# Kernel tuning notes

Measured on AMD Instinct MI355X. Metric: run time of the kernel, lower is better.

## Reference

```python
import jax, jax.numpy as jnp
import numpy as np

# 8 directional difference stencils (N, S, E, W, NE, SE, SW, NW), OIHW [8,1,3,3]
_WINDOWS = np.array([
    [[0, 1, 0], [0, -1, 0], [0, 0, 0]],
    [[0, 0, 0], [0, -1, 0], [0, 1, 0]],
    [[0, 0, 0], [0, -1, 1], [0, 0, 0]],
    [[0, 0, 0], [1, -1, 0], [0, 0, 0]],
    [[0, 0, 1], [0, -1, 0], [0, 0, 0]],
    [[0, 0, 0], [0, -1, 0], [0, 0, 1]],
    [[0, 0, 0], [0, -1, 0], [1, 0, 0]],
    [[1, 0, 0], [0, -1, 0], [0, 0, 0]],
], dtype=np.float32).reshape(8, 1, 3, 3)

ITERATIONS = 30  # int(self.iterations.item()) with init value 30.0


def setup_inputs() -> dict:
    key = jax.random.key(0)
    k1, k2, k3 = jax.random.split(key, 3)
    x = jax.random.normal(k1, (32, 3, 512, 512), dtype=jnp.float32)
    W_expand = jax.random.normal(k2, (3, 3, 1, 1), dtype=jnp.float32) * 0.3
    b_expand = jax.random.normal(k3, (3,), dtype=jnp.float32) * 0.1
    return {
        "x": x,
        "delta": jnp.float32(0.1),
        "kappa": jnp.float32(15.0),
        "W_expand": W_expand,
        "b_expand": b_expand,
    }


def reference(x, delta, kappa, W_expand, b_expand):
    K = jnp.asarray(_WINDOWS)  # [8,1,3,3]
    # axial directions weight 1, diagonal directions weight 1/(sqrt(2))^2 = 0.5
    dir_w = jnp.array([1.0, 1.0, 1.0, 1.0, 0.5, 0.5, 0.5, 0.5],
                      dtype=x.dtype).reshape(1, 8, 1, 1)

    # RGB -> luminance, [B,1,H,W]
    u = (0.299 * x[:, 0] + 0.587 * x[:, 1] + 0.114 * x[:, 2])[:, None]

    def step(u, _):
        # all 8 directional gradients in one grouped conv: [B,8,H,W]
        nabla = jax.lax.conv_general_dilated(
            u, K, window_strides=(1, 1), padding='SAME',
            dimension_numbers=('NCHW', 'OIHW', 'NCHW'))
        diff = 1.0 / (1.0 + (nabla / kappa) ** 2)  # Perona-Malik diffusivity
        upd = jnp.sum(dir_w * diff * nabla, axis=1, keepdims=True)
        return u + delta * upd, None

    u, _ = jax.lax.scan(step, u, None, length=ITERATIONS)

    # repeat to 3 channels then 1x1 conv (expand_channels)
    u_rgb = jnp.repeat(u, 3, axis=1)  # [B,3,H,W]
    out = jnp.einsum('oi,bihw->bohw', W_expand[:, :, 0, 0], u_rgb)
    out = out + b_expand[None, :, None, None]
    return out
```

## Files before the change

kernel.cpp:

```cpp
#include <hip/hip_runtime.h>

#define BATCH 32
#define HGT 512
#define WID 512
#define PLANE (HGT * WID)
#define NPIX (BATCH * PLANE)
#define BSTRIDE (3 * PLANE)
#define NQUAD (NPIX / 4)

#define RSLAB 32
#define SLABS (HGT / RSLAB)
#define FBLOCKS (BATCH * SLABS)
#define FT 512
#define NW 8

__device__ __forceinline__ float4 ld4(const float* p) {
    return *reinterpret_cast<const float4*>(p);
}
__device__ __forceinline__ void st4(float* p, float4 v) {
    *reinterpret_cast<float4*>(p) = v;
}

__device__ __forceinline__ float pm_flux(float d, float ik2) {
    return d * __builtin_amdgcn_rcpf(fmaf(d * d, ik2, 1.f));
}

__device__ __forceinline__ void level_flux(const float a[6], const float b[6],
                                           float vF[4], float seF[5], float swF[5],
                                           float ik2) {
#pragma unroll
    for (int j = 0; j < 4; ++j) vF[j] = pm_flux(b[j + 1] - a[j + 1], ik2);
#pragma unroll
    for (int i = 0; i < 5; ++i) seF[i] = pm_flux(b[i + 1] - a[i], ik2);
#pragma unroll
    for (int i = 0; i < 5; ++i) swF[i] = pm_flux(b[i] - a[i + 1], ik2);
}

__device__ __forceinline__ void load_row2(const float* __restrict__ buf, int row, int o,
                                          float rA[6], float rB[6]) {
    const float* p = buf + row * WID + (o << 2);
    float4 a = ld4(p);
    float4 b = ld4(p + 256);
    float aW63 = __shfl(a.w, 63);
    float bX0  = __shfl(b.x, 0);
    float lA   = __shfl_up(a.w, 1);
    float rAr  = __shfl_down(a.x, 1);
    float lB   = __shfl_up(b.w, 1);
    float rBr  = __shfl_down(b.x, 1);
    rA[0] = (o == 0) ? 0.f : lA;
    rA[1] = a.x; rA[2] = a.y; rA[3] = a.z; rA[4] = a.w;
    rA[5] = (o == 63) ? bX0 : rAr;
    rB[0] = (o == 0) ? aW63 : lB;
    rB[1] = b.x; rB[2] = b.y; rB[3] = b.z; rB[4] = b.w;
    rB[5] = (o == 63) ? 0.f : rBr;
}

struct SegState {
    float m[6];
    float pV[4], pSE[5], pSW[5];
};

__device__ __forceinline__ void seg_init(SegState& S_, const float a6[6],
                                         const float m6[6], float ik2) {
#pragma unroll
    for (int t = 0; t < 6; ++t) S_.m[t] = m6[t];
    level_flux(a6, m6, S_.pV, S_.pSE, S_.pSW, ik2);
}

__device__ __forceinline__ float4 seg_step(SegState& S_, const float d6[6],
                                           float delta, float ik2) {
    float hF[5];
#pragma unroll
    for (int t = 0; t < 5; ++t) hF[t] = pm_flux(S_.m[t + 1] - S_.m[t], ik2);
    float cV[4], cSE[5], cSW[5];
    level_flux(S_.m, d6, cV, cSE, cSW, ik2);
    float o[4];
#pragma unroll
    for (int j = 0; j < 4; ++j) {
        float axial = cV[j] - S_.pV[j] + hF[j + 1] - hF[j];
        float diag  = cSE[j + 1] + cSW[j] - S_.pSE[j] - S_.pSW[j + 1];
        o[j] = fmaf(delta, fmaf(0.5f, diag, axial), S_.m[j + 1]);
    }
#pragma unroll
    for (int t = 0; t < 6; ++t) S_.m[t] = d6[t];
#pragma unroll
    for (int j = 0; j < 4; ++j) S_.pV[j] = cV[j];
#pragma unroll
    for (int t = 0; t < 5; ++t) { S_.pSE[t] = cSE[t]; S_.pSW[t] = cSW[t]; }
    return make_float4(o[0], o[1], o[2], o[3]);
}

template <int MODE, int S>
__global__ __launch_bounds__(FT, 4)
void pm_fusedk(const float* __restrict__ src, int sstr,
               float* __restrict__ dst, int dstr,
               const float* __restrict__ pdelta, const float* __restrict__ pkappa,
               const float* __restrict__ Wexp, const float* __restrict__ bexp) {
    constexpr int LR = RSLAB + 2 * S;
    __shared__ float buf[LR * WID];

    const int img   = blockIdx.x >> 4;
    const int slab  = blockIdx.x & (SLABS - 1);
    const int H0    = slab * RSLAB;
    const int tid   = threadIdx.x;
    const int strip = tid >> 6;
    const int o     = tid & 63;

    const float delta = *pdelta;
    const float kappa = *pkappa;
    const float ik2 = __builtin_amdgcn_rcpf(kappa * kappa);

    const float* sb = src + (size_t)img * sstr;
    for (int i = tid; i < LR * (WID / 4); i += FT) {
        int row = i >> 7;
        int q   = i & 127;
        int g = H0 - S + row;
        float4 v = make_float4(0.f, 0.f, 0.f, 0.f);
        if ((unsigned)g < (unsigned)HGT) {
            const float* p = sb + g * WID + (q << 2);
            if (MODE == 0) {
                float4 r = ld4(p), gg = ld4(p + PLANE), bb = ld4(p + 2 * PLANE);
                v.x = fmaf(0.299f, r.x, fmaf(0.587f, gg.x, 0.114f * bb.x));
                v.y = fmaf(0.299f, r.y, fmaf(0.587f, gg.y, 0.114f * bb.y));
                v.z = fmaf(0.299f, r.z, fmaf(0.587f, gg.z, 0.114f * bb.z));
                v.w = fmaf(0.299f, r.w, fmaf(0.587f, gg.w, 0.114f * bb.w));
            } else {
                v = ld4(p);
            }
        }
        st4(buf + row * WID + (q << 2), v);
    }
    __syncthreads();

    float s0c = 0.f, s1c = 0.f, s2c = 0.f, b0c = 0.f, b1c = 0.f, b2c = 0.f;
    if (MODE == 2) {
        s0c = Wexp[0] + Wexp[1] + Wexp[2];
        s1c = Wexp[3] + Wexp[4] + Wexp[5];
        s2c = Wexp[6] + Wexp[7] + Wexp[8];
        b0c = bexp[0]; b1c = bexp[1]; b2c = bexp[2];
    }

    float* db = dst + (size_t)img * dstr;

    for (int s = 0; s < S; ++s) {
        const int tot = LR - 2 - 2 * s;
        const int bse = tot >> 3, rem = tot & 7;
        const int n   = bse + (strip < rem ? 1 : 0);
        const int st0 = s + 1 + strip * bse + (strip < rem ? strip : rem);
        const bool fin = (s == S - 1);

        SegState SA, SB;
        {
            float a6[6], b6[6], mA[6], mB[6];
            load_row2(buf, st0 - 1, o, a6, b6);
            load_row2(buf, st0, o, mA, mB);
            seg_init(SA, a6, mA, ik2);
            seg_init(SB, b6, mB, ik2);
        }
        float4 fA = make_float4(0, 0, 0, 0), fB = fA, lA4 = fA, lB4 = fA;

        for (int i = 0; i < n; ++i) {
            float dA[6], dB[6];
            load_row2(buf, st0 + i + 1, o, dA, dB);
            float4 rA = seg_step(SA, dA, delta, ik2);
            float4 rB = seg_step(SB, dB, delta, ik2);
            const int g = H0 - S + st0 + i;
            if ((unsigned)g >= (unsigned)HGT) {
                rA = make_float4(0, 0, 0, 0);
                rB = make_float4(0, 0, 0, 0);
            }
            if (fin) {
                float* p = db + (size_t)g * WID + (o << 2);
                if (MODE == 2) {
                    st4(p, make_float4(fmaf(s0c, rA.x, b0c), fmaf(s0c, rA.y, b0c),
                                       fmaf(s0c, rA.z, b0c), fmaf(s0c, rA.w, b0c)));
                    st4(p + 256, make_float4(fmaf(s0c, rB.x, b0c), fmaf(s0c, rB.y, b0c),
                                             fmaf(s0c, rB.z, b0c), fmaf(s0c, rB.w, b0c)));
                    st4(p + PLANE,
                        make_float4(fmaf(s1c, rA.x, b1c), fmaf(s1c, rA.y, b1c),
                                    fmaf(s1c, rA.z, b1c), fmaf(s1c, rA.w, b1c)));
                    st4(p + PLANE + 256,
                        make_float4(fmaf(s1c, rB.x, b1c), fmaf(s1c, rB.y, b1c),
                                    fmaf(s1c, rB.z, b1c), fmaf(s1c, rB.w, b1c)));
                    st4(p + 2 * PLANE,
                        make_float4(fmaf(s2c, rA.x, b2c), fmaf(s2c, rA.y, b2c),
                                    fmaf(s2c, rA.z, b2c), fmaf(s2c, rA.w, b2c)));
                    st4(p + 2 * PLANE + 256,
                        make_float4(fmaf(s2c, rB.x, b2c), fmaf(s2c, rB.y, b2c),
                                    fmaf(s2c, rB.z, b2c), fmaf(s2c, rB.w, b2c)));
                } else {
                    st4(p, rA);
                    st4(p + 256, rB);
                }
            } else if (i == 0) {
                fA = rA; fB = rB;
            } else if (i == n - 1) {
                lA4 = rA; lB4 = rB;
            } else {
                float* p = buf + (st0 + i) * WID + (o << 2);
                st4(p, rA);
                st4(p + 256, rB);
            }
        }
        if (!fin) {
            __syncthreads();
            {
                float* p = buf + st0 * WID + (o << 2);
                st4(p, fA);
                st4(p + 256, fB);
            }
            {
                float* p = buf + (st0 + n - 1) * WID + (o << 2);
                st4(p, lA4);
                st4(p + 256, lB4);
            }
            __syncthreads();
        }
    }
}

__global__ void expand_from(const float* __restrict__ usrc, int ustr,
                            float* __restrict__ out,
                            const float* __restrict__ Wexp,
                            const float* __restrict__ bexp) {
    int idx = blockIdx.x * blockDim.x + threadIdx.x;
    if (idx >= NQUAD) return;
    int b = idx / (PLANE / 4);
    int off = (idx - b * (PLANE / 4)) * 4;

    float4 u = ld4(usrc + (size_t)b * ustr + off);
    float s0 = Wexp[0] + Wexp[1] + Wexp[2];
    float s1 = Wexp[3] + Wexp[4] + Wexp[5];
    float s2 = Wexp[6] + Wexp[7] + Wexp[8];
    float b0 = bexp[0], b1 = bexp[1], b2 = bexp[2];

    size_t base = (size_t)b * BSTRIDE + off;
    st4(out + base, make_float4(fmaf(s0, u.x, b0), fmaf(s0, u.y, b0),
                                fmaf(s0, u.z, b0), fmaf(s0, u.w, b0)));
    st4(out + base + PLANE, make_float4(fmaf(s1, u.x, b1), fmaf(s1, u.y, b1),
                                        fmaf(s1, u.z, b1), fmaf(s1, u.w, b1)));
    st4(out + base + 2 * PLANE, make_float4(fmaf(s2, u.x, b2), fmaf(s2, u.y, b2),
                                            fmaf(s2, u.z, b2), fmaf(s2, u.w, b2)));
}

extern "C" void kernel_launch(void* const* d_in, const int* in_sizes, int n_in,
                              void* d_out, int out_size, void* d_ws, size_t ws_size,
                              hipStream_t stream) {
    const float* x      = (const float*)d_in[0];
    const float* pdelta = (const float*)d_in[1];
    const float* pkappa = (const float*)d_in[2];
    const float* Wexp   = (const float*)d_in[3];
    const float* bexp   = (const float*)d_in[4];
    float* out = (float*)d_out;

    const size_t need = (size_t)2 * NPIX * sizeof(float);
    if (ws_size >= need) {
        float* uA = (float*)d_ws;
        float* uB = uA + NPIX;
        pm_fusedk<0, 4><<<FBLOCKS, FT, 0, stream>>>(
            x, BSTRIDE, uA, PLANE, pdelta, pkappa, Wexp, bexp);
        float* s = uA;
        float* d = uB;
        for (int k = 0; k < 6; ++k) {
            pm_fusedk<1, 4><<<FBLOCKS, FT, 0, stream>>>(
                s, PLANE, d, PLANE, pdelta, pkappa, Wexp, bexp);
            float* t = s; s = d; d = t;
        }
        pm_fusedk<2, 2><<<FBLOCKS, FT, 0, stream>>>(
            s, PLANE, out, BSTRIDE, pdelta, pkappa, Wexp, bexp);
    } else {
        float* uA = out;
        float* uB = out + PLANE;
        pm_fusedk<0, 4><<<FBLOCKS, FT, 0, stream>>>(
            x, BSTRIDE, uA, BSTRIDE, pdelta, pkappa, Wexp, bexp);
        float* s = uA;
        float* d = uB;
        for (int k = 0; k < 6; ++k) {
            pm_fusedk<1, 4><<<FBLOCKS, FT, 0, stream>>>(
                s, BSTRIDE, d, BSTRIDE, pdelta, pkappa, Wexp, bexp);
            float* t = s; s = d; d = t;
        }
        pm_fusedk<1, 2><<<FBLOCKS, FT, 0, stream>>>(
            s, BSTRIDE, d, BSTRIDE, pdelta, pkappa, Wexp, bexp);
        const int block = 256;
        const int grid_q = (NQUAD + block - 1) / block;
        expand_from<<<grid_q, block, 0, stream>>>(d, BSTRIDE, out, Wexp, bexp);
    }
}
```

Measured before the change: 395.9 us.

## Give each lane 8 contiguous columns and ping-pong row state buffers

Each lane now handles 8 contiguous pixels per row instead of two 4-pixel segments 256 columns apart. This cuts the per-row shuffles to two and shares horizontal flux work across a wider run of pixels. The row loop is unrolled by two, alternating two state structs so no register copies are needed. Launch bounds become an explicit waves-per-EU attribute. The stride-8 LDS float4 accesses may cause bank conflicts, and the wider per-thread state raises register pressure.

```diff
diff --git a/kernel.cpp b/kernel.cpp
--- a/kernel.cpp
+++ b/kernel.cpp
@@ -25,73 +25,37 @@
     return d * __builtin_amdgcn_rcpf(fmaf(d * d, ik2, 1.f));
 }
 
-__device__ __forceinline__ void level_flux(const float a[6], const float b[6],
-                                           float vF[4], float seF[5], float swF[5],
-                                           float ik2) {
-#pragma unroll
-    for (int j = 0; j < 4; ++j) vF[j] = pm_flux(b[j + 1] - a[j + 1], ik2);
-#pragma unroll
-    for (int i = 0; i < 5; ++i) seF[i] = pm_flux(b[i + 1] - a[i], ik2);
-#pragma unroll
-    for (int i = 0; i < 5; ++i) swF[i] = pm_flux(b[i] - a[i + 1], ik2);
-}
-
-__device__ __forceinline__ void load_row2(const float* __restrict__ buf, int row, int o,
-                                          float rA[6], float rB[6]) {
-    const float* p = buf + row * WID + (o << 2);
-    float4 a = ld4(p);
-    float4 b = ld4(p + 256);
-    float aW63 = __shfl(a.w, 63);
-    float bX0  = __shfl(b.x, 0);
-    float lA   = __shfl_up(a.w, 1);
-    float rAr  = __shfl_down(a.x, 1);
-    float lB   = __shfl_up(b.w, 1);
-    float rBr  = __shfl_down(b.x, 1);
-    rA[0] = (o == 0) ? 0.f : lA;
-    rA[1] = a.x; rA[2] = a.y; rA[3] = a.z; rA[4] = a.w;
-    rA[5] = (o == 63) ? bX0 : rAr;
-    rB[0] = (o == 0) ? aW63 : lB;
-    rB[1] = b.x; rB[2] = b.y; rB[3] = b.z; rB[4] = b.w;
-    rB[5] = (o == 63) ? 0.f : rBr;
-}
-
-struct SegState {
-    float m[6];
-    float pV[4], pSE[5], pSW[5];
+struct RowState {
+    float m[10];
+    float pV[8], pSE[9], pSW[9];
 };
 
-__device__ __forceinline__ void seg_init(SegState& S_, const float a6[6],
-                                         const float m6[6], float ik2) {
-#pragma unroll
-    for (int t = 0; t < 6; ++t) S_.m[t] = m6[t];
-    level_flux(a6, m6, S_.pV, S_.pSE, S_.pSW, ik2);
-}
-
-__device__ __forceinline__ float4 seg_step(SegState& S_, const float d6[6],
-                                           float delta, float ik2) {
-    float hF[5];
-#pragma unroll
-    for (int t = 0; t < 5; ++t) hF[t] = pm_flux(S_.m[t + 1] - S_.m[t], ik2);
-    float cV[4], cSE[5], cSW[5];
-    level_flux(S_.m, d6, cV, cSE, cSW, ik2);
-    float o[4];
-#pragma unroll
-    for (int j = 0; j < 4; ++j) {
-        float axial = cV[j] - S_.pV[j] + hF[j + 1] - hF[j];
-        float diag  = cSE[j + 1] + cSW[j] - S_.pSE[j] - S_.pSW[j + 1];
-        o[j] = fmaf(delta, fmaf(0.5f, diag, axial), S_.m[j + 1]);
-    }
-#pragma unroll
-    for (int t = 0; t < 6; ++t) S_.m[t] = d6[t];
-#pragma unroll
-    for (int j = 0; j < 4; ++j) S_.pV[j] = cV[j];
-#pragma unroll
-    for (int t = 0; t < 5; ++t) { S_.pSE[t] = cSE[t]; S_.pSW[t] = cSW[t]; }
-    return make_float4(o[0], o[1], o[2], o[3]);
+__device__ __forceinline__ void load_row10(const float* __restrict__ buf, int row, int o,
+                                           float m[10]) {
+    const float* p = buf + row * WID + (o << 3);
+    float4 lo = ld4(p);
+    float4 hi = ld4(p + 4);
+    float le = __shfl_up(hi.w, 1);
+    float re = __shfl_down(lo.x, 1);
+    m[0] = (o == 0) ? 0.f : le;
+    m[1] = lo.x; m[2] = lo.y; m[3] = lo.z; m[4] = lo.w;
+    m[5] = hi.x; m[6] = hi.y; m[7] = hi.z; m[8] = hi.w;
+    m[9] = (o == 63) ? 0.f : re;
+}
+
+__device__ __forceinline__ void level10(const float a[10], const float b[10],
+                                        float vF[8], float seF[9], float swF[9],
+                                        float ik2) {
+#pragma unroll
+    for (int j = 0; j < 8; ++j) vF[j] = pm_flux(b[j + 1] - a[j + 1], ik2);
+#pragma unroll
+    for (int i = 0; i < 9; ++i) seF[i] = pm_flux(b[i + 1] - a[i], ik2);
+#pragma unroll
+    for (int i = 0; i < 9; ++i) swF[i] = pm_flux(b[i] - a[i + 1], ik2);
 }
 
 template <int MODE, int S>
-__global__ __launch_bounds__(FT, 4)
+__global__ __launch_bounds__(FT) __attribute__((amdgpu_waves_per_eu(4, 4)))
 void pm_fusedk(const float* __restrict__ src, int sstr,
                float* __restrict__ dst, int dstr,
                const float* __restrict__ pdelta, const float* __restrict__ pkappa,
@@ -99,12 +63,12 @@
     constexpr int LR = RSLAB + 2 * S;
     __shared__ float buf[LR * WID];
 
-    const int img   = blockIdx.x >> 4;
-    const int slab  = blockIdx.x & (SLABS - 1);
-    const int H0    = slab * RSLAB;
-    const int tid   = threadIdx.x;
-    const int strip = tid >> 6;
-    const int o     = tid & 63;
+    const int img  = blockIdx.x >> 4;
+    const int slab = blockIdx.x & (SLABS - 1);
+    const int H0   = slab * RSLAB;
+    const int tid  = threadIdx.x;
+    const int wave = tid >> 6;
+    const int o    = tid & 63;
 
     const float delta = *pdelta;
     const float kappa = *pkappa;
@@ -145,75 +109,87 @@
     for (int s = 0; s < S; ++s) {
         const int tot = LR - 2 - 2 * s;
         const int bse = tot >> 3, rem = tot & 7;
-        const int n   = bse + (strip < rem ? 1 : 0);
-        const int st0 = s + 1 + strip * bse + (strip < rem ? strip : rem);
+        const int n   = bse + (wave < rem ? 1 : 0);
+        const int st0 = s + 1 + wave * bse + (wave < rem ? wave : rem);
         const bool fin = (s == S - 1);
 
-        SegState SA, SB;
+        RowState A, B;
         {
-            float a6[6], b6[6], mA[6], mB[6];
-            load_row2(buf, st0 - 1, o, a6, b6);
-            load_row2(buf, st0, o, mA, mB);
-            seg_init(SA, a6, mA, ik2);
-            seg_init(SB, b6, mB, ik2);
-        }
-        float4 fA = make_float4(0, 0, 0, 0), fB = fA, lA4 = fA, lB4 = fA;
-
-        for (int i = 0; i < n; ++i) {
-            float dA[6], dB[6];
-            load_row2(buf, st0 + i + 1, o, dA, dB);
-            float4 rA = seg_step(SA, dA, delta, ik2);
-            float4 rB = seg_step(SB, dB, delta, ik2);
+            float a10[10];
+            load_row10(buf, st0 - 1, o, a10);
+            load_row10(buf, st0, o, A.m);
+            level10(a10, A.m, A.pV, A.pSE, A.pSW, ik2);
+        }
+        float4 f0 = make_float4(0, 0, 0, 0), f1 = f0, l0 = f0, l1 = f0;
+
+        auto do_row = [&](RowState& CUR, RowState& NEXT, int i) {
+            load_row10(buf, st0 + i + 1, o, NEXT.m);
+            float hF[9];
+#pragma unroll
+            for (int t = 0; t < 9; ++t) hF[t] = pm_flux(CUR.m[t + 1] - CUR.m[t], ik2);
+            level10(CUR.m, NEXT.m, NEXT.pV, NEXT.pSE, NEXT.pSW, ik2);
+            float o8[8];
+#pragma unroll
+            for (int j = 0; j < 8; ++j) {
+                float axial = NEXT.pV[j] - CUR.pV[j] + hF[j + 1] - hF[j];
+                float diag  = NEXT.pSE[j + 1] + NEXT.pSW[j]
+                            - CUR.pSE[j] - CUR.pSW[j + 1];
+                o8[j] = fmaf(delta, fmaf(0.5f, diag, axial), CUR.m[j + 1]);
+            }
             const int g = H0 - S + st0 + i;
             if ((unsigned)g >= (unsigned)HGT) {
-                rA = make_float4(0, 0, 0, 0);
-                rB = make_float4(0, 0, 0, 0);
-            }
+#pragma unroll
+                for (int j = 0; j < 8; ++j) o8[j] = 0.f;
+            }
+            float4 r0 = make_float4(o8[0], o8[1], o8[2], o8[3]);
+            float4 r1 = make_float4(o8[4], o8[5], o8[6], o8[7]);
             if (fin) {
-                float* p = db + (size_t)g * WID + (o << 2);
+                float* p = db + (size_t)g * WID + (o << 3);
                 if (MODE == 2) {
-                    st4(p, make_float4(fmaf(s0c, rA.x, b0c), fmaf(s0c, rA.y, b0c),
-                                       fmaf(s0c, rA.z, b0c), fmaf(s0c, rA.w, b0c)));
-                    st4(p + 256, make_float4(fmaf(s0c, rB.x, b0c), fmaf(s0c, rB.y, b0c),
-                                             fmaf(s0c, rB.z, b0c), fmaf(s0c, rB.w, b0c)));
+                    st4(p, make_float4(fmaf(s0c, r0.x, b0c), fmaf(s0c, r0.y, b0c),
+                                       fmaf(s0c, r0.z, b0c), fmaf(s0c, r0.w, b0c)));
+                    st4(p + 4, make_float4(fmaf(s0c, r1.x, b0c), fmaf(s0c, r1.y, b0c),
+                                           fmaf(s0c, r1.z, b0c), fmaf(s0c, r1.w, b0c)));
                     st4(p + PLANE,
-                        make_float4(fmaf(s1c, rA.x, b1c), fmaf(s1c, rA.y, b1c),
-                                    fmaf(s1c, rA.z, b1c), fmaf(s1c, rA.w, b1c)));
-                    st4(p + PLANE + 256,
-                        make_float4(fmaf(s1c, rB.x, b1c), fmaf(s1c, rB.y, b1c),
-                                    fmaf(s1c, rB.z, b1c), fmaf(s1c, rB.w, b1c)));
+                        make_float4(fmaf(s1c, r0.x, b1c), fmaf(s1c, r0.y, b1c),
+                                    fmaf(s1c, r0.z, b1c), fmaf(s1c, r0.w, b1c)));
+                    st4(p + PLANE + 4,
+                        make_float4(fmaf(s1c, r1.x, b1c), fmaf(s1c, r1.y, b1c),
+                                    fmaf(s1c, r1.z, b1c), fmaf(s1c, r1.w, b1c)));
                     st4(p + 2 * PLANE,
-                        make_float4(fmaf(s2c, rA.x, b2c), fmaf(s2c, rA.y, b2c),
-                                    fmaf(s2c, rA.z, b2c), fmaf(s2c, rA.w, b2c)));
-                    st4(p + 2 * PLANE + 256,
-                        make_float4(fmaf(s2c, rB.x, b2c), fmaf(s2c, rB.y, b2c),
-                                    fmaf(s2c, rB.z, b2c), fmaf(s2c, rB.w, b2c)));
+                        make_float4(fmaf(s2c, r0.x, b2c), fmaf(s2c, r0.y, b2c),
+                                    fmaf(s2c, r0.z, b2c), fmaf(s2c, r0.w, b2c)));
+                    st4(p + 2 * PLANE + 4,
+                        make_float4(fmaf(s2c, r1.x, b2c), fmaf(s2c, r1.y, b2c),
+                                    fmaf(s2c, r1.z, b2c), fmaf(s2c, r1.w, b2c)));
                 } else {
-                    st4(p, rA);
-                    st4(p + 256, rB);
+                    st4(p, r0);
+                    st4(p + 4, r1);
                 }
             } else if (i == 0) {
-                fA = rA; fB = rB;
+                f0 = r0; f1 = r1;
             } else if (i == n - 1) {
-                lA4 = rA; lB4 = rB;
+                l0 = r0; l1 = r1;
             } else {
-                float* p = buf + (st0 + i) * WID + (o << 2);
-                st4(p, rA);
-                st4(p + 256, rB);
-            }
-        }
+                float* p = buf + (st0 + i) * WID + (o << 3);
+                st4(p, r0);
+                st4(p + 4, r1);
+            }
+        };
+
+        for (int i = 0; i < n; i += 2) {
+            do_row(A, B, i);
+            if (i + 1 < n) do_row(B, A, i + 1);
+        }
+
         if (!fin) {
             __syncthreads();
-            {
-                float* p = buf + st0 * WID + (o << 2);
-                st4(p, fA);
-                st4(p + 256, fB);
-            }
-            {
-                float* p = buf + (st0 + n - 1) * WID + (o << 2);
-                st4(p, lA4);
-                st4(p + 256, lB4);
-            }
+            float* p = buf + st0 * WID + (o << 3);
+            st4(p, f0);
+            st4(p + 4, f1);
+            p = buf + (st0 + n - 1) * WID + (o << 3);
+            st4(p, l0);
+            st4(p + 4, l1);
             __syncthreads();
         }
     }
```

Measured after the change: 378.3 us. -4.4%, faster.
